# Kernel tuning notes

Hardware: AMD Instinct MI355X
Metric: run time of the kernel (lower is better)

## Reference

```python
import jax, jax.numpy as jnp
import numpy as np
from jax import lax

N = 100000   # num_nodes
E = 1600000  # num_edges (avg degree 16)
F = 128      # num_features
H = 256      # hidden_channels
C = 64       # num_classes
K = 10       # propagation steps
ALPHA = 0.1
BETA = 0.5
THETA = 0.5
EPS = 1e-5   # BatchNorm eps


def setup_inputs() -> dict:
    key = jax.random.key(0)
    ks = jax.random.split(key, 16)
    x = jax.random.normal(ks[0], (N, F), dtype=jnp.float32)
    src = jax.random.randint(ks[1], (E,), 0, N, dtype=jnp.int32)
    dst = jax.random.randint(ks[2], (E,), 0, N, dtype=jnp.int32)
    # row-normalized adjacency weights so repeated A@z stays bounded
    deg = jax.ops.segment_sum(jnp.ones((E,), jnp.float32), dst, num_segments=N)
    w = (1.0 / jnp.maximum(deg, 1.0))[dst]
    # MLP params (Linear + BatchNorm per hidden layer)
    W1 = jax.random.normal(ks[3], (F, H), dtype=jnp.float32) * 0.05
    b1 = jnp.zeros((H,), jnp.float32)
    g1 = jnp.ones((H,), jnp.float32)
    be1 = jnp.zeros((H,), jnp.float32)
    W2 = jax.random.normal(ks[4], (H, H), dtype=jnp.float32) * 0.05
    b2 = jnp.zeros((H,), jnp.float32)
    g2 = jnp.ones((H,), jnp.float32)
    be2 = jnp.zeros((H,), jnp.float32)
    W3 = jax.random.normal(ks[5], (H, C), dtype=jnp.float32) * 0.05
    b3 = jnp.zeros((C,), jnp.float32)
    # lazy caches (warm-start memories); nonzero so the blend branch is taken
    z_sam = jax.random.normal(ks[6], (N, C), dtype=jnp.float32) * 0.1
    g_sam = jax.random.normal(ks[7], (N, C), dtype=jnp.float32) * 0.01
    return dict(x=x, src=src, dst=dst, w=w,
                W1=W1, b1=b1, g1=g1, be1=be1,
                W2=W2, b2=b2, g2=g2, be2=be2,
                W3=W3, b3=b3, z_sam=z_sam, g_sam=g_sam, size=N)


def _bn(h, gamma, beta):
    # BatchNorm1d in training mode: batch statistics over nodes
    mu = jnp.mean(h, axis=0)
    var = jnp.var(h, axis=0)
    return (h - mu) * jax.lax.rsqrt(var + EPS) * gamma + beta


def reference(x, src, dst, w, W1, b1, g1, be1, W2, b2, g2, be2, W3, b3,
              z_sam, g_sam, size):
    # MLP stack: Linear -> BN -> ReLU (dropout omitted: deterministic reference)
    h = jax.nn.relu(_bn(x @ W1 + b1, g1, be1))
    h = jax.nn.relu(_bn(h @ W2 + b2, g2, be2))
    logits = h @ W3 + b3  # [N, C]

    def spmm(z):
        # (A @ z)_i = sum_{j -> i} w_ij * z_j
        return jax.ops.segment_sum(z[src] * w[:, None], dst, num_segments=N)

    # Lazy_Prop.forward: warm-start blend, then K propagation steps
    use_x = jnp.all(z_sam[:size] == 0.0)
    z0 = jnp.where(use_x, logits, (1.0 - BETA) * z_sam + BETA * logits)
    z = lax.fori_loop(0, K, lambda i, z: (1.0 - ALPHA) * spmm(z) + ALPHA * logits, z0)
    return jax.nn.log_softmax(z, axis=1)
```

## Files before the change

### kernel.cpp

```cpp
#include <hip/hip_runtime.h>
#include <hip/hip_bf16.h>

#define NODES 100000
#define EDGES 1600000
#define FEAT  128
#define HID   256
#define CLS   64
#define KPROP 10
#define ALPHA_C 0.1f
#define BETA_C  0.5f
#define BN_EPS  1e-5f

typedef __attribute__((ext_vector_type(8))) short short8;
typedef __attribute__((ext_vector_type(4))) float f32x4;

static __device__ __forceinline__ unsigned short f2b(float f) {
    __hip_bfloat16 h = __float2bfloat16(f);
    return *(unsigned short*)&h;
}
static __device__ __forceinline__ float b2f(unsigned short u) {
    __hip_bfloat16 h;
    *(unsigned short*)&h = u;
    return __bfloat162float(h);
}
static __device__ __forceinline__ float asf(unsigned int u) {
    union { unsigned int u; float f; } c; c.u = u; return c.f;
}

__global__ void packwt_k(const float* __restrict__ W, unsigned short* __restrict__ Wt,
                         int K, int N)
{
    int i = blockIdx.x * 256 + threadIdx.x;
    if (i < K * N) {
        int k = i / N, n = i - k * N;
        Wt[(size_t)n * K + k] = f2b(W[i]);
    }
}

template<bool AF32, bool FUSE, bool STATS, bool OUTF32, int KK, bool COLSPLIT>
__global__ __launch_bounds__(256, 2)
void gemm_stream_k(const void* __restrict__ Ain, const unsigned short* __restrict__ Wt,
                   const float* __restrict__ bias,
                   const float* __restrict__ scale, const float* __restrict__ shift,
                   void* __restrict__ outp,
                   float* __restrict__ gsum, float* __restrict__ gsq,
                   int M, int N)
{
    const int lane = threadIdx.x & 63;
    const int wv   = threadIdx.x >> 6;
    const int quad = lane >> 4;
    const int l16  = lane & 15;
    constexpr int NK8 = KK / 32;

    int rbase, colbase;
    if constexpr (COLSPLIT) { rbase = blockIdx.x * 32;             colbase = wv * 64; }
    else                    { rbase = (blockIdx.x * 4 + wv) * 32;  colbase = 0;       }

    short8 Bf[4][NK8];
    #pragma unroll
    for (int ct = 0; ct < 4; ++ct) {
        const unsigned short* wp = Wt + (size_t)(colbase + ct * 16 + l16) * KK + quad * 8;
        #pragma unroll
        for (int ks = 0; ks < NK8; ++ks)
            Bf[ct][ks] = *(const short8*)(wp + ks * 32);
    }

    f32x4 acc[2][4];
    #pragma unroll
    for (int i = 0; i < 2; ++i)
        #pragma unroll
        for (int j = 0; j < 4; ++j)
            acc[i][j] = (f32x4){0.f, 0.f, 0.f, 0.f};

    #pragma unroll
    for (int ks = 0; ks < NK8; ++ks) {
        const int k = ks * 32 + quad * 8;
        float sc[8], sh[8];
        if constexpr (FUSE) {
            float4 s0 = *(const float4*)(scale + k);
            float4 s1 = *(const float4*)(scale + k + 4);
            float4 h0 = *(const float4*)(shift + k);
            float4 h1 = *(const float4*)(shift + k + 4);
            sc[0]=s0.x; sc[1]=s0.y; sc[2]=s0.z; sc[3]=s0.w;
            sc[4]=s1.x; sc[5]=s1.y; sc[6]=s1.z; sc[7]=s1.w;
            sh[0]=h0.x; sh[1]=h0.y; sh[2]=h0.z; sh[3]=h0.w;
            sh[4]=h1.x; sh[5]=h1.y; sh[6]=h1.z; sh[7]=h1.w;
        }
        short8 a[2];
        #pragma unroll
        for (int rt = 0; rt < 2; ++rt) {
            int row = rbase + rt * 16 + l16;
            float v[8];
            if (row < M) {
                if constexpr (AF32) {
                    const float* ap = (const float*)Ain + (size_t)row * KK + k;
                    float4 t0 = *(const float4*)ap;
                    float4 t1 = *(const float4*)(ap + 4);
                    v[0]=t0.x; v[1]=t0.y; v[2]=t0.z; v[3]=t0.w;
                    v[4]=t1.x; v[5]=t1.y; v[6]=t1.z; v[7]=t1.w;
                } else {
                    short8 t = *(const short8*)((const unsigned short*)Ain + (size_t)row * KK + k);
                    #pragma unroll
                    for (int j = 0; j < 8; ++j) v[j] = b2f((unsigned short)t[j]);
                }
            } else {
                #pragma unroll
                for (int j = 0; j < 8; ++j) v[j] = 0.f;
            }
            if constexpr (FUSE) {
                #pragma unroll
                for (int j = 0; j < 8; ++j) v[j] = fmaxf(fmaf(v[j], sc[j], sh[j]), 0.f);
            }
            short8 av;
            #pragma unroll
            for (int j = 0; j < 8; ++j) av[j] = (short)f2b(v[j]);
            a[rt] = av;
        }
        #pragma unroll
        for (int ct = 0; ct < 4; ++ct) {
            acc[0][ct] = __builtin_amdgcn_mfma_f32_16x16x32_bf16(a[0], Bf[ct][ks], acc[0][ct], 0, 0, 0);
            acc[1][ct] = __builtin_amdgcn_mfma_f32_16x16x32_bf16(a[1], Bf[ct][ks], acc[1][ct], 0, 0, 0);
        }
    }

    float ps[4] = {0.f, 0.f, 0.f, 0.f};
    float pq[4] = {0.f, 0.f, 0.f, 0.f};
    #pragma unroll
    for (int ct = 0; ct < 4; ++ct) {
        int col = colbase + ct * 16 + l16;
        float bcol = bias[col];
        #pragma unroll
        for (int rt = 0; rt < 2; ++rt) {
            #pragma unroll
            for (int r2 = 0; r2 < 4; ++r2) {
                int row = rbase + rt * 16 + quad * 4 + r2;
                float v = acc[rt][ct][r2] + bcol;
                if (row < M) {
                    if constexpr (STATS) { ps[ct] += v; pq[ct] += v * v; }
                    if constexpr (OUTF32) {
                        ((float*)outp)[(size_t)row * N + col] = v;
                    } else {
                        ((unsigned short*)outp)[(size_t)row * N + col] = f2b(v);
                    }
                }
            }
        }
    }
    if constexpr (STATS) {
        #pragma unroll
        for (int ct = 0; ct < 4; ++ct) {
            float s = ps[ct];
            s += __shfl_xor(s, 16, 64);
            s += __shfl_xor(s, 32, 64);
            float q = pq[ct];
            q += __shfl_xor(q, 16, 64);
            q += __shfl_xor(q, 32, 64);
            if (lane < 16) {
                atomicAdd(&gsum[colbase + ct * 16 + lane], s);
                atomicAdd(&gsq[colbase + ct * 16 + lane], q);
            }
        }
    }
}

__global__ void bnfin_k(const float* __restrict__ sum, const float* __restrict__ sq,
                        const float* __restrict__ g, const float* __restrict__ be,
                        float* __restrict__ scale, float* __restrict__ shift)
{
    int c = threadIdx.x;
    float mu = sum[c] * (1.f / NODES);
    float var = sq[c] * (1.f / NODES) - mu * mu;
    float sc = g[c] * rsqrtf(var + BN_EPS);
    scale[c] = sc;
    shift[c] = be[c] - mu * sc;
}

__global__ void flag_k(const float* __restrict__ zs, int* __restrict__ flag)
{
    int i = blockIdx.x * 256 + threadIdx.x;
    bool nz = (i < NODES * CLS) && (zs[i] != 0.f);
    if (__any(nz)) {
        if ((threadIdx.x & 63) == 0) *flag = 1;
    }
}

__global__ void blend_k(const float* __restrict__ zs, const float* __restrict__ logits,
                        const int* __restrict__ flag, unsigned short* __restrict__ z0)
{
    int i = blockIdx.x * 256 + threadIdx.x;
    if (i < NODES * CLS) {
        float l = logits[i];
        float v = (*flag) ? ((1.f - BETA_C) * zs[i] + BETA_C * l) : l;
        z0[i] = f2b(v);
    }
}

__global__ void count_k(const int* __restrict__ dst, int* __restrict__ cnt)
{
    int i = blockIdx.x * 256 + threadIdx.x;
    if (i < EDGES) atomicAdd(&cnt[dst[i]], 1);
}

__global__ void scan1_k(const int* __restrict__ cnt, int* __restrict__ rowptr,
                        int* __restrict__ bsum)
{
    __shared__ int s[256];
    int tid = threadIdx.x;
    int i = blockIdx.x * 256 + tid;
    int v = (i < NODES) ? cnt[i] : 0;
    s[tid] = v;
    __syncthreads();
    for (int off = 1; off < 256; off <<= 1) {
        int t = (tid >= off) ? s[tid - off] : 0;
        __syncthreads();
        s[tid] += t;
        __syncthreads();
    }
    if (i < NODES) rowptr[i] = s[tid] - v;
    if (tid == 255) bsum[blockIdx.x] = s[255];
}

__global__ void scan2_k(const int* __restrict__ bsum, int* __restrict__ boffs, int nb)
{
    __shared__ int s[512];
    int tid = threadIdx.x;
    int v = (tid < nb) ? bsum[tid] : 0;
    s[tid] = v;
    __syncthreads();
    for (int off = 1; off < 512; off <<= 1) {
        int t = (tid >= off) ? s[tid - off] : 0;
        __syncthreads();
        s[tid] += t;
        __syncthreads();
    }
    if (tid < nb) boffs[tid] = s[tid] - v;
}

__global__ void scan3_k(int* __restrict__ rowptr, const int* __restrict__ boffs,
                        int* __restrict__ cursor)
{
    int i = blockIdx.x * 256 + threadIdx.x;
    if (i < NODES) {
        int v = rowptr[i] + boffs[blockIdx.x];
        rowptr[i] = v;
        cursor[i] = v;
    }
    if (i == 0) rowptr[NODES] = EDGES;
}

__global__ void fill_k(const int* __restrict__ src, const int* __restrict__ dst,
                       int* __restrict__ cursor, int* __restrict__ esrc)
{
    int i = blockIdx.x * 256 + threadIdx.x;
    if (i < EDGES) {
        int pos = atomicAdd(&cursor[dst[i]], 1);
        esrc[pos] = src[i];
    }
}

__global__ __launch_bounds__(256)
void prop_k(const int* __restrict__ rowptr, const int* __restrict__ esrc,
            const unsigned int* __restrict__ zin, const float* __restrict__ logits,
            unsigned int* __restrict__ zout)
{
    int row = blockIdx.x * 8 + (threadIdx.x >> 5);
    if (row >= NODES) return;
    int l32 = threadIdx.x & 31;
    int beg = rowptr[row], end = rowptr[row + 1];
    float acc0 = 0.f, acc1 = 0.f;

    for (int cbeg = beg; cbeg < end; cbeg += 32) {
        int e = cbeg + l32;
        int s_l = (e < end) ? esrc[e] : 0;
        int cnt = min(32, end - cbeg);
        int j = 0;
        for (; j + 8 <= cnt; j += 8) {
            int idx[8];
            #pragma unroll
            for (int u = 0; u < 8; ++u) idx[u] = __shfl(s_l, j + u, 32);
            unsigned int vv[8];
            #pragma unroll
            for (int u = 0; u < 8; ++u)
                vv[u] = __hip_atomic_load(zin + (size_t)idx[u] * 32 + l32,
                                          __ATOMIC_RELAXED, __HIP_MEMORY_SCOPE_AGENT);
            #pragma unroll
            for (int u = 0; u < 8; ++u) {
                acc0 += asf(vv[u] << 16);
                acc1 += asf(vv[u] & 0xffff0000u);
            }
        }
        for (; j < cnt; ++j) {
            int s0 = __shfl(s_l, j, 32);
            unsigned int v = __hip_atomic_load(zin + (size_t)s0 * 32 + l32,
                                               __ATOMIC_RELAXED, __HIP_MEMORY_SCOPE_AGENT);
            acc0 += asf(v << 16);
            acc1 += asf(v & 0xffff0000u);
        }
    }
    float dg = (float)(end - beg);
    float inv = 1.f / fmaxf(dg, 1.f);
    float2 lv = *(const float2*)(logits + (size_t)row * CLS + l32 * 2);
    float r0 = (1.f - ALPHA_C) * inv * acc0 + ALPHA_C * lv.x;
    float r1 = (1.f - ALPHA_C) * inv * acc1 + ALPHA_C * lv.y;
    zout[(size_t)row * 32 + l32] = ((unsigned int)f2b(r1) << 16) | (unsigned int)f2b(r0);
}

__global__ __launch_bounds__(256)
void logsoftmax_k(const unsigned short* __restrict__ z, float* __restrict__ out)
{
    int row = blockIdx.x * 4 + (threadIdx.x >> 6);
    if (row >= NODES) return;
    int lane = threadIdx.x & 63;
    float v = b2f(z[(size_t)row * CLS + lane]);
    float m = v;
    #pragma unroll
    for (int off = 32; off > 0; off >>= 1) m = fmaxf(m, __shfl_xor(m, off, 64));
    float ex = expf(v - m);
    float s = ex;
    #pragma unroll
    for (int off = 32; off > 0; off >>= 1) s += __shfl_xor(s, off, 64);
    out[(size_t)row * CLS + lane] = (v - m) - logf(s);
}

extern "C" void kernel_launch(void* const* d_in, const int* in_sizes, int n_in,
                              void* d_out, int out_size, void* d_ws, size_t ws_size,
                              hipStream_t stream)
{
    const float* x   = (const float*)d_in[0];
    const int*   src = (const int*)d_in[1];
    const int*   dst = (const int*)d_in[2];
    const float* W1  = (const float*)d_in[4];
    const float* b1  = (const float*)d_in[5];
    const float* g1  = (const float*)d_in[6];
    const float* be1 = (const float*)d_in[7];
    const float* W2  = (const float*)d_in[8];
    const float* b2  = (const float*)d_in[9];
    const float* g2  = (const float*)d_in[10];
    const float* be2 = (const float*)d_in[11];
    const float* W3  = (const float*)d_in[12];
    const float* b3  = (const float*)d_in[13];
    const float* zsam = (const float*)d_in[14];
    float* outp = (float*)d_out;

    uint8_t* base = (uint8_t*)d_ws;
    float* s_scale1 = (float*)(base);
    float* s_shift1 = s_scale1 + 256;
    float* s_scale2 = s_shift1 + 256;
    float* s_shift2 = s_scale2 + 256;
    float* s_sum    = s_shift2 + 256;
    float* s_sq     = s_sum + 256;
    int*   flag     = (int*)(s_sq + 256);

    unsigned short* Wt1 = (unsigned short*)(base + (1 << 14));
    unsigned short* Wt2 = Wt1 + (size_t)FEAT * HID;
    unsigned short* Wt3 = Wt2 + (size_t)HID * HID;
    unsigned short* h1  = Wt3 + (size_t)HID * CLS;
    unsigned short* h2  = h1 + (size_t)NODES * HID;
    float* logits = (float*)(h2 + (size_t)NODES * HID);
    unsigned short* zA  = (unsigned short*)(logits + (size_t)NODES * CLS);
    unsigned short* zB  = zA + (size_t)NODES * CLS;
    int* esrc   = (int*)(zB + (size_t)NODES * CLS);
    int* rowptr = esrc + EDGES;
    int* cursor = rowptr + (NODES + 1);
    int* cnt    = cursor + NODES;
    int* bsum   = cnt + NODES;
    int* boffs  = bsum + 512;

    const int STRIPS = (NODES + 31) / 32;
    const int SCANB  = (NODES + 255) / 256;

    packwt_k<<<(FEAT * HID + 255) / 256, 256, 0, stream>>>(W1, Wt1, FEAT, HID);
    packwt_k<<<(HID * HID + 255) / 256, 256, 0, stream>>>(W2, Wt2, HID, HID);
    packwt_k<<<(HID * CLS + 255) / 256, 256, 0, stream>>>(W3, Wt3, HID, CLS);

    hipMemsetAsync(cnt, 0, NODES * sizeof(int), stream);
    count_k<<<(EDGES + 255) / 256, 256, 0, stream>>>(dst, cnt);
    scan1_k<<<SCANB, 256, 0, stream>>>(cnt, rowptr, bsum);
    scan2_k<<<1, 512, 0, stream>>>(bsum, boffs, SCANB);
    scan3_k<<<SCANB, 256, 0, stream>>>(rowptr, boffs, cursor);
    fill_k<<<(EDGES + 255) / 256, 256, 0, stream>>>(src, dst, cursor, esrc);

    hipMemsetAsync(s_sum, 0, 512 * sizeof(float), stream);
    gemm_stream_k<true, false, true, false, FEAT, true><<<STRIPS, 256, 0, stream>>>(
        x, Wt1, b1, nullptr, nullptr, h1, s_sum, s_sq, NODES, HID);
    bnfin_k<<<1, 256, 0, stream>>>(s_sum, s_sq, g1, be1, s_scale1, s_shift1);

    hipMemsetAsync(s_sum, 0, 512 * sizeof(float), stream);
    gemm_stream_k<false, true, true, false, HID, true><<<STRIPS, 256, 0, stream>>>(
        h1, Wt2, b2, s_scale1, s_shift1, h2, s_sum, s_sq, NODES, HID);
    bnfin_k<<<1, 256, 0, stream>>>(s_sum, s_sq, g2, be2, s_scale2, s_shift2);

    gemm_stream_k<false, true, false, true, HID, false><<<(STRIPS + 3) / 4, 256, 0, stream>>>(
        h2, Wt3, b3, s_scale2, s_shift2, logits, nullptr, nullptr, NODES, CLS);

    hipMemsetAsync(flag, 0, sizeof(int), stream);
    flag_k<<<(NODES * CLS + 255) / 256, 256, 0, stream>>>(zsam, flag);
    blend_k<<<(NODES * CLS + 255) / 256, 256, 0, stream>>>(zsam, logits, flag, zA);

    const int PROPB = (NODES + 7) / 8;
    for (int it = 0; it < KPROP; ++it) {
        const unsigned int* zi = (const unsigned int*)((it & 1) ? zB : zA);
        unsigned int* zo = (unsigned int*)((it & 1) ? zA : zB);
        prop_k<<<PROPB, 256, 0, stream>>>(rowptr, esrc, zi, logits, zo);
    }

    logsoftmax_k<<<(NODES + 3) / 4, 256, 0, stream>>>(zA, outp);
}
```

Baseline: 1.023 ms.

## Stage GEMM weights in LDS with 2D tiling and widen SpMM to 16 lanes per row

The MLP GEMM now uses a 2D grid of 128-row by 64-column tiles. Each block stages its 64-column weight slice and the BN scale/shift into shared memory, and prefetches all A fragments into registers before the MFMA loop. This replaces holding every weight fragment in registers, aiming to cut register pressure and raise occupancy (launch bounds go from 2 to 3). The propagation kernel now uses 16 lanes per row, each loading 64-bit (4 bf16) words, to halve per-row lanes and widen gathers. The costs are extra LDS traffic, redundant A reads across column blocks, and possibly more register use from the prefetched A arrays.

```diff
diff --git a/kernel.cpp b/kernel.cpp
--- a/kernel.cpp
+++ b/kernel.cpp
@@ -37,8 +37,8 @@
     }
 }
 
-template<bool AF32, bool FUSE, bool STATS, bool OUTF32, int KK, bool COLSPLIT>
-__global__ __launch_bounds__(256, 2)
+template<bool AF32, bool FUSE, bool STATS, bool OUTF32, int KK>
+__global__ __launch_bounds__(256, 3)
 void gemm_stream_k(const void* __restrict__ Ain, const unsigned short* __restrict__ Wt,
                    const float* __restrict__ bias,
                    const float* __restrict__ scale, const float* __restrict__ shift,
@@ -46,23 +46,54 @@
                    float* __restrict__ gsum, float* __restrict__ gsq,
                    int M, int N)
 {
-    const int lane = threadIdx.x & 63;
-    const int wv   = threadIdx.x >> 6;
+    constexpr int NK8 = KK / 32;
+    constexpr int KP  = KK + 8;
+    __shared__ unsigned short Ws[64 * KP];
+    __shared__ float scs[KK];
+    __shared__ float shs[KK];
+
+    const int tid  = threadIdx.x;
+    const int lane = tid & 63;
+    const int wv   = tid >> 6;
     const int quad = lane >> 4;
     const int l16  = lane & 15;
-    constexpr int NK8 = KK / 32;
-
-    int rbase, colbase;
-    if constexpr (COLSPLIT) { rbase = blockIdx.x * 32;             colbase = wv * 64; }
-    else                    { rbase = (blockIdx.x * 4 + wv) * 32;  colbase = 0;       }
-
-    short8 Bf[4][NK8];
-    #pragma unroll
-    for (int ct = 0; ct < 4; ++ct) {
-        const unsigned short* wp = Wt + (size_t)(colbase + ct * 16 + l16) * KK + quad * 8;
-        #pragma unroll
-        for (int ks = 0; ks < NK8; ++ks)
-            Bf[ct][ks] = *(const short8*)(wp + ks * 32);
+    const int m0   = blockIdx.x * 128;
+    const int n0   = blockIdx.y * 64;
+
+    {
+        int r  = tid >> 2;
+        int c0 = (tid & 3) * (KK / 4);
+        #pragma unroll
+        for (int p = 0; p < KK / 4; p += 8)
+            *(short8*)&Ws[r * KP + c0 + p] =
+                *(const short8*)(Wt + (size_t)(n0 + r) * KK + c0 + p);
+        if constexpr (FUSE) {
+            if (tid < KK) { scs[tid] = scale[tid]; shs[tid] = shift[tid]; }
+        }
+    }
+    __syncthreads();
+
+    const int rowb = m0 + wv * 32;
+    bool ok[2];
+    ok[0] = rowb + l16 < M;
+    ok[1] = rowb + 16 + l16 < M;
+    short8 araw16[2][NK8];
+    float4 araw32[2][NK8][2];
+    #pragma unroll
+    for (int rt = 0; rt < 2; ++rt) {
+        int arow = rowb + rt * 16 + l16;
+        if (arow >= M) arow = M - 1;
+        #pragma unroll
+        for (int ks = 0; ks < NK8; ++ks) {
+            int k = ks * 32 + quad * 8;
+            if constexpr (AF32) {
+                const float* ap = (const float*)Ain + (size_t)arow * KK + k;
+                araw32[rt][ks][0] = *(const float4*)ap;
+                araw32[rt][ks][1] = *(const float4*)(ap + 4);
+            } else {
+                araw16[rt][ks] = *(const short8*)((const unsigned short*)Ain + (size_t)arow * KK + k);
+            }
+        }
     }
 
     f32x4 acc[2][4];
@@ -75,41 +106,36 @@
     #pragma unroll
     for (int ks = 0; ks < NK8; ++ks) {
         const int k = ks * 32 + quad * 8;
-        float sc[8], sh[8];
+        float sc8[8], sh8[8];
         if constexpr (FUSE) {
-            float4 s0 = *(const float4*)(scale + k);
-            float4 s1 = *(const float4*)(scale + k + 4);
-            float4 h0 = *(const float4*)(shift + k);
-            float4 h1 = *(const float4*)(shift + k + 4);
-            sc[0]=s0.x; sc[1]=s0.y; sc[2]=s0.z; sc[3]=s0.w;
-            sc[4]=s1.x; sc[5]=s1.y; sc[6]=s1.z; sc[7]=s1.w;
-            sh[0]=h0.x; sh[1]=h0.y; sh[2]=h0.z; sh[3]=h0.w;
-            sh[4]=h1.x; sh[5]=h1.y; sh[6]=h1.z; sh[7]=h1.w;
+            float4 s0 = *(const float4*)&scs[k];
+            float4 s1 = *(const float4*)&scs[k + 4];
+            float4 h0 = *(const float4*)&shs[k];
+            float4 h1 = *(const float4*)&shs[k + 4];
+            sc8[0]=s0.x; sc8[1]=s0.y; sc8[2]=s0.z; sc8[3]=s0.w;
+            sc8[4]=s1.x; sc8[5]=s1.y; sc8[6]=s1.z; sc8[7]=s1.w;
+            sh8[0]=h0.x; sh8[1]=h0.y; sh8[2]=h0.z; sh8[3]=h0.w;
+            sh8[4]=h1.x; sh8[5]=h1.y; sh8[6]=h1.z; sh8[7]=h1.w;
         }
         short8 a[2];
         #pragma unroll
         for (int rt = 0; rt < 2; ++rt) {
-            int row = rbase + rt * 16 + l16;
             float v[8];
-            if (row < M) {
-                if constexpr (AF32) {
-                    const float* ap = (const float*)Ain + (size_t)row * KK + k;
-                    float4 t0 = *(const float4*)ap;
-                    float4 t1 = *(const float4*)(ap + 4);
-                    v[0]=t0.x; v[1]=t0.y; v[2]=t0.z; v[3]=t0.w;
-                    v[4]=t1.x; v[5]=t1.y; v[6]=t1.z; v[7]=t1.w;
-                } else {
-                    short8 t = *(const short8*)((const unsigned short*)Ain + (size_t)row * KK + k);
-                    #pragma unroll
-                    for (int j = 0; j < 8; ++j) v[j] = b2f((unsigned short)t[j]);
-                }
+            if constexpr (AF32) {
+                float4 t0 = araw32[rt][ks][0], t1 = araw32[rt][ks][1];
+                v[0]=t0.x; v[1]=t0.y; v[2]=t0.z; v[3]=t0.w;
+                v[4]=t1.x; v[5]=t1.y; v[6]=t1.z; v[7]=t1.w;
             } else {
                 #pragma unroll
+                for (int j = 0; j < 8; ++j) v[j] = b2f((unsigned short)araw16[rt][ks][j]);
+            }
+            if (!ok[rt]) {
+                #pragma unroll
                 for (int j = 0; j < 8; ++j) v[j] = 0.f;
             }
             if constexpr (FUSE) {
                 #pragma unroll
-                for (int j = 0; j < 8; ++j) v[j] = fmaxf(fmaf(v[j], sc[j], sh[j]), 0.f);
+                for (int j = 0; j < 8; ++j) v[j] = fmaxf(fmaf(v[j], sc8[j], sh8[j]), 0.f);
             }
             short8 av;
             #pragma unroll
@@ -118,8 +144,9 @@
         }
         #pragma unroll
         for (int ct = 0; ct < 4; ++ct) {
-            acc[0][ct] = __builtin_amdgcn_mfma_f32_16x16x32_bf16(a[0], Bf[ct][ks], acc[0][ct], 0, 0, 0);
-            acc[1][ct] = __builtin_amdgcn_mfma_f32_16x16x32_bf16(a[1], Bf[ct][ks], acc[1][ct], 0, 0, 0);
+            short8 b = *(const short8*)&Ws[(ct * 16 + l16) * KP + k];
+            acc[0][ct] = __builtin_amdgcn_mfma_f32_16x16x32_bf16(a[0], b, acc[0][ct], 0, 0, 0);
+            acc[1][ct] = __builtin_amdgcn_mfma_f32_16x16x32_bf16(a[1], b, acc[1][ct], 0, 0, 0);
         }
     }
 
@@ -127,13 +154,13 @@
     float pq[4] = {0.f, 0.f, 0.f, 0.f};
     #pragma unroll
     for (int ct = 0; ct < 4; ++ct) {
-        int col = colbase + ct * 16 + l16;
+        int col = n0 + ct * 16 + l16;
         float bcol = bias[col];
         #pragma unroll
         for (int rt = 0; rt < 2; ++rt) {
             #pragma unroll
             for (int r2 = 0; r2 < 4; ++r2) {
-                int row = rbase + rt * 16 + quad * 4 + r2;
+                int row = rowb + rt * 16 + quad * 4 + r2;
                 float v = acc[rt][ct][r2] + bcol;
                 if (row < M) {
                     if constexpr (STATS) { ps[ct] += v; pq[ct] += v * v; }
@@ -156,8 +183,8 @@
             q += __shfl_xor(q, 16, 64);
             q += __shfl_xor(q, 32, 64);
             if (lane < 16) {
-                atomicAdd(&gsum[colbase + ct * 16 + lane], s);
-                atomicAdd(&gsq[colbase + ct * 16 + lane], q);
+                atomicAdd(&gsum[n0 + ct * 16 + lane], s);
+                atomicAdd(&gsq[n0 + ct * 16 + lane], q);
             }
         }
     }
@@ -260,49 +287,63 @@
 
 __global__ __launch_bounds__(256)
 void prop_k(const int* __restrict__ rowptr, const int* __restrict__ esrc,
-            const unsigned int* __restrict__ zin, const float* __restrict__ logits,
-            unsigned int* __restrict__ zout)
-{
-    int row = blockIdx.x * 8 + (threadIdx.x >> 5);
+            const unsigned long long* __restrict__ zin,
+            const float* __restrict__ logits,
+            unsigned long long* __restrict__ zout)
+{
+    int t = blockIdx.x * 256 + threadIdx.x;
+    int row = t >> 4;
     if (row >= NODES) return;
-    int l32 = threadIdx.x & 31;
+    int l16 = threadIdx.x & 15;
     int beg = rowptr[row], end = rowptr[row + 1];
-    float acc0 = 0.f, acc1 = 0.f;
-
-    for (int cbeg = beg; cbeg < end; cbeg += 32) {
-        int e = cbeg + l32;
+    float a0 = 0.f, a1 = 0.f, a2 = 0.f, a3 = 0.f;
+
+    for (int cbeg = beg; cbeg < end; cbeg += 16) {
+        int e = cbeg + l16;
         int s_l = (e < end) ? esrc[e] : 0;
-        int cnt = min(32, end - cbeg);
+        int cnt = min(16, end - cbeg);
         int j = 0;
         for (; j + 8 <= cnt; j += 8) {
             int idx[8];
             #pragma unroll
-            for (int u = 0; u < 8; ++u) idx[u] = __shfl(s_l, j + u, 32);
-            unsigned int vv[8];
+            for (int u = 0; u < 8; ++u) idx[u] = __shfl(s_l, j + u, 16);
+            unsigned long long vv[8];
             #pragma unroll
             for (int u = 0; u < 8; ++u)
-                vv[u] = __hip_atomic_load(zin + (size_t)idx[u] * 32 + l32,
+                vv[u] = __hip_atomic_load(zin + (size_t)idx[u] * 16 + l16,
                                           __ATOMIC_RELAXED, __HIP_MEMORY_SCOPE_AGENT);
             #pragma unroll
             for (int u = 0; u < 8; ++u) {
-                acc0 += asf(vv[u] << 16);
-                acc1 += asf(vv[u] & 0xffff0000u);
+                unsigned int lo = (unsigned int)vv[u];
+                unsigned int hi = (unsigned int)(vv[u] >> 32);
+                a0 += asf(lo << 16);
+                a1 += asf(lo & 0xffff0000u);
+                a2 += asf(hi << 16);
+                a3 += asf(hi & 0xffff0000u);
             }
         }
         for (; j < cnt; ++j) {
-            int s0 = __shfl(s_l, j, 32);
-            unsigned int v = __hip_atomic_load(zin + (size_t)s0 * 32 + l32,
-                                               __ATOMIC_RELAXED, __HIP_MEMORY_SCOPE_AGENT);
-            acc0 += asf(v << 16);
-            acc1 += asf(v & 0xffff0000u);
+            int s0 = __shfl(s_l, j, 16);
+            unsigned long long v = __hip_atomic_load(zin + (size_t)s0 * 16 + l16,
+                                                     __ATOMIC_RELAXED, __HIP_MEMORY_SCOPE_AGENT);
+            unsigned int lo = (unsigned int)v;
+            unsigned int hi = (unsigned int)(v >> 32);
+            a0 += asf(lo << 16);
+            a1 += asf(lo & 0xffff0000u);
+            a2 += asf(hi << 16);
+            a3 += asf(hi & 0xffff0000u);
         }
     }
     float dg = (float)(end - beg);
     float inv = 1.f / fmaxf(dg, 1.f);
-    float2 lv = *(const float2*)(logits + (size_t)row * CLS + l32 * 2);
-    float r0 = (1.f - ALPHA_C) * inv * acc0 + ALPHA_C * lv.x;
-    float r1 = (1.f - ALPHA_C) * inv * acc1 + ALPHA_C * lv.y;
-    zout[(size_t)row * 32 + l32] = ((unsigned int)f2b(r1) << 16) | (unsigned int)f2b(r0);
+    float4 lv = *(const float4*)(logits + (size_t)row * CLS + l16 * 4);
+    float r0 = (1.f - ALPHA_C) * inv * a0 + ALPHA_C * lv.x;
+    float r1 = (1.f - ALPHA_C) * inv * a1 + ALPHA_C * lv.y;
+    float r2 = (1.f - ALPHA_C) * inv * a2 + ALPHA_C * lv.z;
+    float r3 = (1.f - ALPHA_C) * inv * a3 + ALPHA_C * lv.w;
+    unsigned int lo = ((unsigned int)f2b(r1) << 16) | (unsigned int)f2b(r0);
+    unsigned int hi = ((unsigned int)f2b(r3) << 16) | (unsigned int)f2b(r2);
+    zout[(size_t)row * 16 + l16] = ((unsigned long long)hi << 32) | lo;
 }
 
 __global__ __launch_bounds__(256)
@@ -366,8 +407,8 @@
     int* bsum   = cnt + NODES;
     int* boffs  = bsum + 512;
 
-    const int STRIPS = (NODES + 31) / 32;
-    const int SCANB  = (NODES + 255) / 256;
+    const int MROWG = (NODES + 127) / 128;
+    const int SCANB = (NODES + 255) / 256;
 
     packwt_k<<<(FEAT * HID + 255) / 256, 256, 0, stream>>>(W1, Wt1, FEAT, HID);
     packwt_k<<<(HID * HID + 255) / 256, 256, 0, stream>>>(W2, Wt2, HID, HID);
@@ -381,26 +422,26 @@
     fill_k<<<(EDGES + 255) / 256, 256, 0, stream>>>(src, dst, cursor, esrc);
 
     hipMemsetAsync(s_sum, 0, 512 * sizeof(float), stream);
-    gemm_stream_k<true, false, true, false, FEAT, true><<<STRIPS, 256, 0, stream>>>(
+    gemm_stream_k<true, false, true, false, FEAT><<<dim3(MROWG, HID / 64), 256, 0, stream>>>(
         x, Wt1, b1, nullptr, nullptr, h1, s_sum, s_sq, NODES, HID);
     bnfin_k<<<1, 256, 0, stream>>>(s_sum, s_sq, g1, be1, s_scale1, s_shift1);
 
     hipMemsetAsync(s_sum, 0, 512 * sizeof(float), stream);
-    gemm_stream_k<false, true, true, false, HID, true><<<STRIPS, 256, 0, stream>>>(
+    gemm_stream_k<false, true, true, false, HID><<<dim3(MROWG, HID / 64), 256, 0, stream>>>(
         h1, Wt2, b2, s_scale1, s_shift1, h2, s_sum, s_sq, NODES, HID);
     bnfin_k<<<1, 256, 0, stream>>>(s_sum, s_sq, g2, be2, s_scale2, s_shift2);
 
-    gemm_stream_k<false, true, false, true, HID, false><<<(STRIPS + 3) / 4, 256, 0, stream>>>(
+    gemm_stream_k<false, true, false, true, HID><<<dim3(MROWG, 1), 256, 0, stream>>>(
         h2, Wt3, b3, s_scale2, s_shift2, logits, nullptr, nullptr, NODES, CLS);
 
     hipMemsetAsync(flag, 0, sizeof(int), stream);
     flag_k<<<(NODES * CLS + 255) / 256, 256, 0, stream>>>(zsam, flag);
     blend_k<<<(NODES * CLS + 255) / 256, 256, 0, stream>>>(zsam, logits, flag, zA);
 
-    const int PROPB = (NODES + 7) / 8;
+    const int PROPB = (NODES * 16 + 255) / 256;
     for (int it = 0; it < KPROP; ++it) {
-        const unsigned int* zi = (const unsigned int*)((it & 1) ? zB : zA);
-        unsigned int* zo = (unsigned int*)((it & 1) ? zA : zB);
+        const unsigned long long* zi = (const unsigned long long*)((it & 1) ? zB : zA);
+        unsigned long long* zo = (unsigned long long*)((it & 1) ? zA : zB);
         prop_k<<<PROPB, 256, 0, stream>>>(rowptr, esrc, zi, logits, zo);
     }
 
```

Result: slower. 1.173 ms (+14.7%).
